# Kernel tuning notes

Measured on AMD Instinct MI355X. Metric: run time of the kernel, lower is better.

The kernel has to match this reference:

```python
import jax, jax.numpy as jnp
import numpy as np

B, T, TA = 16, 512, 1024
D_REG, D_AUD, HID, HEADS = 512, 512, 256, 4
NREG = 4  # mouth, left_eye, right_eye, nose (dict order)
N = NREG * B * T + B * TA  # total graph nodes


def _build_edges():
    # Faithful, vectorized version of build_graph's edge construction (phoneme_times=None).
    bs = np.arange(B)[:, None]
    ts = np.arange(T)[None, :]
    src, dst = [], []
    # cross-region same-timestep edges, all ordered pairs i != j (edge_attr 0)
    for i in range(NREG):
        for j in range(NREG):
            if i != j:
                n1 = i * B * T + bs * T + ts
                n2 = j * B * T + bs * T + ts
                src.append(n1.ravel()); dst.append(n2.ravel())
    # temporal edges within each region (edge_attr 1)
    tt = np.arange(T - 1)[None, :]
    for i in range(NREG):
        n1 = i * B * T + bs * T + tt
        src.append(n1.ravel()); dst.append((n1 + 1).ravel())
    # eye (region idx 1,2) -> audio alignment edges (edge_attr 3)
    t_aud = (np.arange(T)[None, :] * TA) // T
    audio_start = NREG * B * T
    for i in (1, 2):
        n_eye = i * B * T + bs * T + ts
        n_aud = audio_start + bs * TA + t_aud
        src.append(n_eye.ravel()); dst.append(np.broadcast_to(n_aud, (B, T)).ravel())
    # self loops (PyG GATConv default add_self_loops=True)
    loops = np.arange(N)
    src.append(loops); dst.append(loops)
    return np.concatenate(src).astype(np.int32), np.concatenate(dst).astype(np.int32)


def setup_inputs() -> dict:
    key = jax.random.key(0)
    ks = iter(jax.random.split(key, 48))
    def rn(shape, scale=1.0):
        return jax.random.normal(next(ks), shape, dtype=jnp.float32) * jnp.float32(scale)
    src_np, dst_np = _build_edges()
    inp = {
        'mouth': rn((B, T, D_REG)), 'left_eye': rn((B, T, D_REG)),
        'right_eye': rn((B, T, D_REG)), 'nose': rn((B, T, D_REG)),
        'audio_embeddings': rn((B, TA, D_AUD)),
    }
    s = 1.0 / np.sqrt(D_REG)
    for name in ['mouth', 'left_eye', 'right_eye', 'nose']:
        inp['w_' + name] = rn((D_REG, HID), s)
        inp['b_' + name] = jnp.zeros((HID,), jnp.float32)
    inp['w_audio'] = rn((D_AUD, HID), 1.0 / np.sqrt(D_AUD))
    inp['b_audio'] = jnp.zeros((HID,), jnp.float32)
    # GAT layers: layer 0 in=HID, layers 1,2 in=HID*HEADS; layers 0,1 concat, layer 2 averages heads
    dims_in = [HID, HID * HEADS, HID * HEADS]
    for l, din in enumerate(dims_in):
        concat = l < 2
        inp[f'W{l}'] = rn((din, HEADS * HID), 1.0 / np.sqrt(din))
        inp[f'as{l}'] = rn((HEADS, HID), 0.1)
        inp[f'ad{l}'] = rn((HEADS, HID), 0.1)
        inp[f'bias{l}'] = jnp.zeros((HEADS * HID,) if concat else (HID,), jnp.float32)
    inp['ln_g'] = jnp.ones((HID,), jnp.float32)
    inp['ln_b'] = jnp.zeros((HID,), jnp.float32)
    inp['src'] = jnp.asarray(src_np)
    inp['dst'] = jnp.asarray(dst_np)
    return inp


def _gat(x, W, a_s, a_d, bias, src, dst, concat):
    # PyG GATConv (eval mode): gather -> per-head attention softmax over dst -> scatter-add
    H, C = a_s.shape
    h = (x @ W).reshape(-1, H, C)                      # [N,H,C]
    alpha_s = jnp.sum(h * a_s, -1)                     # [N,H]
    alpha_d = jnp.sum(h * a_d, -1)                     # [N,H]
    e = jax.nn.leaky_relu(alpha_s[src] + alpha_d[dst], 0.2)  # [E,H]
    m = jax.ops.segment_max(e, dst, num_segments=N)
    ex = jnp.exp(e - m[dst])
    denom = jax.ops.segment_sum(ex, dst, num_segments=N)
    alpha = ex / (denom[dst] + jnp.float32(1e-16))
    out = jax.ops.segment_sum(h[src] * alpha[:, :, None], dst, num_segments=N)  # [N,H,C]
    out = out.reshape(-1, H * C) if concat else out.mean(1)
    return out + bias


def _forward(mouth, left_eye, right_eye, nose, audio_embeddings,
             w_mouth, b_mouth, w_left_eye, b_left_eye, w_right_eye, b_right_eye,
             w_nose, b_nose, w_audio, b_audio,
             W0, as0, ad0, bias0, W1, as1, ad1, bias1, W2, as2, ad2, bias2,
             ln_g, ln_b, src, dst):
    x = jnp.concatenate([
        (mouth @ w_mouth + b_mouth).reshape(B * T, HID),
        (left_eye @ w_left_eye + b_left_eye).reshape(B * T, HID),
        (right_eye @ w_right_eye + b_right_eye).reshape(B * T, HID),
        (nose @ w_nose + b_nose).reshape(B * T, HID),
        (audio_embeddings @ w_audio + b_audio).reshape(B * TA, HID),
    ], axis=0)                                          # [N,HID]
    x = _gat(x, W0, as0, ad0, bias0, src, dst, True)    # [N,HID*HEADS]
    x = _gat(x, W1, as1, ad1, bias1, src, dst, True)    # [N,HID*HEADS]
    x = _gat(x, W2, as2, ad2, bias2, src, dst, False)   # [N,HID]
    mu = x.mean(-1, keepdims=True)
    var = jnp.mean(jnp.square(x - mu), -1, keepdims=True)
    x = (x - mu) / jnp.sqrt(var + jnp.float32(1e-5)) * ln_g + ln_b
    nodes_pb = NREG * T + TA
    return x.reshape(B, nodes_pb, HID).mean(1)          # [B,HID]


def reference(mouth, left_eye, right_eye, nose, audio_embeddings,
              w_mouth, b_mouth, w_left_eye, b_left_eye, w_right_eye, b_right_eye,
              w_nose, b_nose, w_audio, b_audio,
              W0, as0, ad0, bias0, W1, as1, ad1, bias1, W2, as2, ad2, bias2,
              ln_g, ln_b, src, dst):
    return _forward(mouth, left_eye, right_eye, nose, audio_embeddings,
                    w_mouth, b_mouth, w_left_eye, b_left_eye, w_right_eye, b_right_eye,
                    w_nose, b_nose, w_audio, b_audio,
                    W0, as0, ad0, bias0, W1, as1, ad1, bias1, W2, as2, ad2, bias2,
                    ln_g, ln_b, src, dst)
```

## Files before the change

kernel.cpp:

```cpp
#include <hip/hip_runtime.h>


typedef unsigned short u16;
typedef unsigned int u32;
typedef __bf16 bf16x8 __attribute__((ext_vector_type(8)));
typedef float f32x4 __attribute__((ext_vector_type(4)));

#define ASYNC16(gp, lp)                                                        \
  __builtin_amdgcn_global_load_lds(                                            \
      (const __attribute__((address_space(1))) void*)(gp),                     \
      (__attribute__((address_space(3))) void*)(lp), 16, 0, 0)

__device__ __forceinline__ u16 f2bf(float f) {
  union { float f; u32 u; } v; v.f = f;
  u32 u = v.u + 0x7FFFu + ((v.u >> 16) & 1u);
  return (u16)(u >> 16);
}
__device__ __forceinline__ float bf2f(u16 x) {
  union { u32 u; float f; } v; v.u = ((u32)x) << 16;
  return v.f;
}
__device__ __forceinline__ float4 cvt4(ushort4 s) {
  float4 r; r.x = bf2f(s.x); r.y = bf2f(s.y); r.z = bf2f(s.z); r.w = bf2f(s.w);
  return r;
}
__device__ __forceinline__ float4 load_bf4(const u16* p) {
  return cvt4(*(const ushort4*)p);
}
__device__ __forceinline__ float lrelu(float v) { return v > 0.f ? v : 0.2f * v; }
__device__ __forceinline__ float dot4(float4 a, float4 b) {
  return a.x * b.x + a.y * b.y + a.z * b.z + a.w * b.w;
}
__device__ __forceinline__ float wredx(float v) {
#pragma unroll
  for (int off = 32; off; off >>= 1) v += __shfl_xor(v, off);
  return v;
}

struct PK { const float* W[8]; u16* P[8]; int KB[8]; int NN[8]; int st[9]; };
__global__ __launch_bounds__(256) void pack_kernel(PK p) {
  const int f = blockIdx.x * 4 + (threadIdx.x >> 6);
  const int lane = threadIdx.x & 63;
  int e = 0;
  while (f >= p.st[e + 1]) ++e;
  const int local = f - p.st[e];
  const int KB = p.KB[e], N = p.NN[e];
  const int nt = local / KB, kb = local % KB;
  const float* W = p.W[e] + (size_t)(kb * 32 + (lane >> 4) * 8) * N + nt * 16 + (lane & 15);
  u16* dst = p.P[e] + ((size_t)local * 64 + lane) * 8;
  u16 o[8];
#pragma unroll
  for (int j = 0; j < 8; ++j) o[j] = f2bf(W[(size_t)j * N]);
  *(uint4*)dst = *(uint4*)o;
}

__global__ __launch_bounds__(256) void gemm_kernel(
    const u16* __restrict__ A, const u16* __restrict__ Bp, u16* __restrict__ C,
    int K, int ldc) {
  __shared__ __align__(16) u16 As[2][2][128 * 32];
  const int KB = K >> 5;
  const int KB2 = K >> 6;
  const int w = blockIdx.y * 8 + blockIdx.x;
  const int xcd = w & 7, m = w >> 3;
  const int blockCol = (m & 7) * 128;
  const int blockRow = ((m >> 3) * 8 + xcd) * 128;
  const int tid = threadIdx.x;
  const int wave = tid >> 6, lane = tid & 63;
  const int wr = (wave >> 1) * 64, wc = (wave & 1) * 64;
  const int lr = lane & 15, lq = lane >> 4;
  const int sRow = wave * 16 + (lane >> 2);
  const int sGc = (lane & 3) ^ ((sRow >> 1) & 3);
  const size_t aOff0 = (size_t)(blockRow + sRow) * K + sGc * 8;
  const size_t aOff1 = aOff0 + (size_t)64 * K;
  const int ldsOff0 = wave * 512;
  const int ldsOff1 = 2048 + wave * 512;

  const u16* Bn[4];
#pragma unroll
  for (int ni = 0; ni < 4; ++ni)
    Bn[ni] = Bp + ((size_t)(((blockCol + wc) >> 4) + ni) * KB) * 512 + lane * 8;

  f32x4 acc[4][4] = {};

#pragma unroll
  for (int h = 0; h < 2; ++h) {
    ASYNC16(A + aOff0 + h * 32, As[0][h] + ldsOff0);
    ASYNC16(A + aOff1 + h * 32, As[0][h] + ldsOff1);
  }
  __syncthreads();

  for (int kb2 = 0; kb2 < KB2; ++kb2) {
    const int cb = kb2 & 1;
    if (kb2 + 1 < KB2) {
      const size_t k1 = (size_t)(kb2 + 1) * 64;
#pragma unroll
      for (int h = 0; h < 2; ++h) {
        ASYNC16(A + aOff0 + k1 + h * 32, As[cb ^ 1][h] + ldsOff0);
        ASYNC16(A + aOff1 + k1 + h * 32, As[cb ^ 1][h] + ldsOff1);
      }
    }
#pragma unroll
    for (int h = 0; h < 2; ++h) {
      const int kb = kb2 * 2 + h;
      const u16* cur = As[cb][h];
      bf16x8 bfr[4];
#pragma unroll
      for (int ni = 0; ni < 4; ++ni)
        bfr[ni] = *(const bf16x8*)(Bn[ni] + (size_t)kb * 512);
      bf16x8 af[4];
#pragma unroll
      for (int mi = 0; mi < 4; ++mi) {
        const int R = wr + mi * 16 + lr;
        const int cp = lq ^ ((R >> 1) & 3);
        af[mi] = *(const bf16x8*)(cur + R * 32 + cp * 8);
      }
#pragma unroll
      for (int mi = 0; mi < 4; ++mi)
#pragma unroll
        for (int ni = 0; ni < 4; ++ni)
          acc[mi][ni] = __builtin_amdgcn_mfma_f32_16x16x32_bf16(af[mi], bfr[ni],
                                                                acc[mi][ni], 0, 0, 0);
    }
    __syncthreads();
  }
#pragma unroll
  for (int mi = 0; mi < 4; ++mi)
#pragma unroll
    for (int ni = 0; ni < 4; ++ni) {
      const int col = blockCol + wc + ni * 16 + lr;
#pragma unroll
      for (int r = 0; r < 4; ++r) {
        const int row = blockRow + wr + mi * 16 + lq * 4 + r;
        C[(size_t)row * ldc + col] = f2bf(acc[mi][ni][r]);
      }
    }
}

struct ProjArgs { const float* x[5]; const u16* w[5]; const float* b[5]; };
__global__ __launch_bounds__(256) void proj_kernel(ProjArgs pa,
                                                   u16* __restrict__ C) {
  __shared__ __align__(16) u16 As[128 * 32];
  const int blockRow = blockIdx.y * 128, blockCol = blockIdx.x * 128;
  const int reg = blockRow >= 32768 ? 4 : (blockRow >> 13);
  const int regBase = reg == 4 ? 32768 : reg * 8192;
  const float* Af = pa.x[reg] + (size_t)(blockRow - regBase) * 512;
  const u16* Bp = pa.w[reg];
  const int tid = threadIdx.x;
  const int wave = tid >> 6, lane = tid & 63;
  const int wr = (wave >> 1) * 64, wc = (wave & 1) * 64;
  const int lr = lane & 15, lq = lane >> 4;
  const int rr = tid >> 2;
  const int cphys = tid & 3;
  const int sGc = cphys ^ ((tid >> 3) & 3);

  const u16* Bn[4];
#pragma unroll
  for (int ni = 0; ni < 4; ++ni)
    Bn[ni] = Bp + ((size_t)(((blockCol + wc) >> 4) + ni) * 16) * 512 + lane * 8;

  f32x4 acc[4][4] = {};

  for (int k0 = 0; k0 < 512; k0 += 32) {
    __syncthreads();
    bf16x8 bfr[4];
#pragma unroll
    for (int ni = 0; ni < 4; ++ni)
      bfr[ni] = *(const bf16x8*)(Bn[ni] + (size_t)k0 * 16);
#pragma unroll
    for (int i = 0; i < 2; ++i) {
      const int row = i * 64 + rr;
      const float* ap = Af + (size_t)row * 512 + k0 + sGc * 8;
      float4 f0 = *(const float4*)(ap);
      float4 f1 = *(const float4*)(ap + 4);
      uint4 pk;
      pk.x = (u32)f2bf(f0.x) | ((u32)f2bf(f0.y) << 16);
      pk.y = (u32)f2bf(f0.z) | ((u32)f2bf(f0.w) << 16);
      pk.z = (u32)f2bf(f1.x) | ((u32)f2bf(f1.y) << 16);
      pk.w = (u32)f2bf(f1.z) | ((u32)f2bf(f1.w) << 16);
      *(uint4*)(&As[row * 32 + cphys * 8]) = pk;
    }
    __syncthreads();
    bf16x8 af[4];
#pragma unroll
    for (int mi = 0; mi < 4; ++mi) {
      const int R = wr + mi * 16 + lr;
      const int cp = lq ^ ((R >> 1) & 3);
      af[mi] = *(const bf16x8*)(&As[R * 32 + cp * 8]);
    }
#pragma unroll
    for (int mi = 0; mi < 4; ++mi)
#pragma unroll
      for (int ni = 0; ni < 4; ++ni)
        acc[mi][ni] = __builtin_amdgcn_mfma_f32_16x16x32_bf16(af[mi], bfr[ni],
                                                              acc[mi][ni], 0, 0, 0);
  }
  const float* bias = pa.b[reg];
#pragma unroll
  for (int mi = 0; mi < 4; ++mi)
#pragma unroll
    for (int ni = 0; ni < 4; ++ni) {
      const int col = blockCol + wc + ni * 16 + lr;
      const float bv = bias[col];
#pragma unroll
      for (int r = 0; r < 4; ++r) {
        const int row = blockRow + wr + mi * 16 + lq * 4 + r;
        C[(size_t)row * 256 + col] = f2bf(acc[mi][ni][r] + bv);
      }
    }
}

template <bool MEAN>
__global__ __launch_bounds__(256) void agg_kernel(
    const u16* __restrict__ h, const float* __restrict__ a_s,
    const float* __restrict__ a_d, const float* __restrict__ bias,
    const float* __restrict__ lng, const float* __restrict__ lnb,
    void* __restrict__ out) {
  const int tid = threadIdx.x;
  const int head = tid >> 6;
  const int c4 = tid * 4;
  const float4 sa = *(const float4*)(a_s + c4);
  const float4 da = *(const float4*)(a_d + c4);

  if (blockIdx.x < 2048) {
    const int b = blockIdx.x >> 7;
    const int t0 = (blockIdx.x & 127) * 4;
    const int btBase = b * 512 + t0;
    float4 hprev[4];
    float ssPrev[4] = {};
    if (t0 > 0) {
#pragma unroll
      for (int r = 0; r < 4; ++r)
        hprev[r] = load_bf4(h + (size_t)(r * 8192 + btBase - 1) * 1024 + c4);
#pragma unroll
      for (int r = 0; r < 4; ++r) ssPrev[r] = wredx(dot4(hprev[r], sa));
    }
    ushort4 rcur[4];
#pragma unroll
    for (int r = 0; r < 4; ++r)
      rcur[r] = *(const ushort4*)(h + (size_t)(r * 8192 + btBase) * 1024 + c4);

    float pacc[4] = {};
    int pch[4] = {-1, -1, -1, -1};

    for (int tt = 0; tt < 4; ++tt) {
      const int bt = btBase + tt;
      const bool hasPrev = (t0 + tt) > 0;
      ushort4 rnxt[4];
      if (tt < 3) {
#pragma unroll
        for (int r = 0; r < 4; ++r)
          rnxt[r] = *(const ushort4*)(h + (size_t)(r * 8192 + bt + 1) * 1024 + c4);
      }
      float4 hv[4];
#pragma unroll
      for (int r = 0; r < 4; ++r) hv[r] = cvt4(rcur[r]);
      float ss[4], dd[4];
#pragma unroll
      for (int r = 0; r < 4; ++r) {
        ss[r] = wredx(dot4(hv[r], sa));
        dd[r] = wredx(dot4(hv[r], da));
      }
      float4 av[4];
#pragma unroll
      for (int j = 0; j < 4; ++j) {
        const float ad = dd[j];
        float e0 = lrelu(ss[0] + ad), e1 = lrelu(ss[1] + ad);
        float e2 = lrelu(ss[2] + ad), e3 = lrelu(ss[3] + ad);
        float mx = fmaxf(fmaxf(e0, e1), fmaxf(e2, e3));
        float e4 = 0.f;
        if (hasPrev) { e4 = lrelu(ssPrev[j] + ad); mx = fmaxf(mx, e4); }
        const float x0 = __expf(e0 - mx), x1 = __expf(e1 - mx);
        const float x2 = __expf(e2 - mx), x3 = __expf(e3 - mx);
        const float x4 = hasPrev ? __expf(e4 - mx) : 0.f;
        const float inv = 1.f / (x0 + x1 + x2 + x3 + x4 + 1e-16f);
        const float a0 = x0 * inv, a1 = x1 * inv, a2 = x2 * inv, a3 = x3 * inv;
        const float a4 = x4 * inv;
        float4 acc;
        acc.x = a0 * hv[0].x + a1 * hv[1].x + a2 * hv[2].x + a3 * hv[3].x;
        acc.y = a0 * hv[0].y + a1 * hv[1].y + a2 * hv[2].y + a3 * hv[3].y;
        acc.z = a0 * hv[0].z + a1 * hv[1].z + a2 * hv[2].z + a3 * hv[3].z;
        acc.w = a0 * hv[0].w + a1 * hv[1].w + a2 * hv[2].w + a3 * hv[3].w;
        if (hasPrev) {
          acc.x += a4 * hprev[j].x; acc.y += a4 * hprev[j].y;
          acc.z += a4 * hprev[j].z; acc.w += a4 * hprev[j].w;
        }
        av[j] = acc;
      }
      if constexpr (!MEAN) {
        const float4 bv = *(const float4*)(bias + c4);
        u16* ob = (u16*)out;
#pragma unroll
        for (int j = 0; j < 4; ++j) {
          ushort4 o;
          o.x = f2bf(av[j].x + bv.x); o.y = f2bf(av[j].y + bv.y);
          o.z = f2bf(av[j].z + bv.z); o.w = f2bf(av[j].w + bv.w);
          *(ushort4*)(ob + (size_t)(j * 8192 + bt) * 1024 + c4) = o;
        }
      } else {
        __shared__ float red[4096];
        __shared__ float ls[32];
#pragma unroll
        for (int j = 0; j < 4; ++j) *(float4*)(&red[j * 1024 + c4]) = av[j];
        __syncthreads();
        const float bb = bias[tid];
        float v[4];
#pragma unroll
        for (int j = 0; j < 4; ++j) {
          v[j] = 0.25f * (red[j * 1024 + tid] + red[j * 1024 + tid + 256] +
                          red[j * 1024 + tid + 512] + red[j * 1024 + tid + 768]) + bb;
          const float sj = wredx(v[j]);
          const float qj = wredx(v[j] * v[j]);
          if ((tid & 63) == 0) { ls[head * 8 + j * 2] = sj; ls[head * 8 + j * 2 + 1] = qj; }
        }
        __syncthreads();
#pragma unroll
        for (int j = 0; j < 4; ++j) {
          const float S = ls[j * 2] + ls[8 + j * 2] + ls[16 + j * 2] + ls[24 + j * 2];
          const float Q = ls[j * 2 + 1] + ls[8 + j * 2 + 1] + ls[16 + j * 2 + 1] +
                          ls[24 + j * 2 + 1];
          const float mean = S * (1.f / 256.f);
          const float var = Q * (1.f / 256.f) - mean * mean;
          const float n = (v[j] - mean) * rsqrtf(var + 1e-5f) * lng[tid] + lnb[tid];
          const int ch = (j * 8192 + bt) / 3072;
          if (ch != pch[j]) {
            if (pch[j] >= 0) atomicAdd((float*)out + pch[j] * 256 + tid, pacc[j]);
            pacc[j] = 0.f; pch[j] = ch;
          }
          pacc[j] += n;
        }
      }
#pragma unroll
      for (int r = 0; r < 4; ++r) {
        hprev[r] = hv[r];
        ssPrev[r] = ss[r];
        rcur[r] = rnxt[r];
      }
    }
    if constexpr (MEAN) {
#pragma unroll
      for (int j = 0; j < 4; ++j)
        if (pch[j] >= 0) atomicAdd((float*)out + pch[j] * 256 + tid, pacc[j]);
    }
  } else {
    const int aid = blockIdx.x - 2048;
    const int idx0 = aid * 2;
    const int b = idx0 >> 10;
    const int ta0 = idx0 & 1023;
    const int n0 = 32768 + idx0, n1 = n0 + 1;
    const int tt2 = ta0 >> 1;
    const int le = 8192 + b * 512 + tt2;
    const int re = 16384 + b * 512 + tt2;
    float4 v0 = load_bf4(h + (size_t)n0 * 1024 + c4);
    float4 vo = load_bf4(h + (size_t)n1 * 1024 + c4);
    float4 v1 = load_bf4(h + (size_t)le * 1024 + c4);
    float4 v2 = load_bf4(h + (size_t)re * 1024 + c4);
    const float s0 = wredx(dot4(v0, sa));
    const float s1 = wredx(dot4(v1, sa));
    const float s2 = wredx(dot4(v2, sa));
    const float d0 = wredx(dot4(v0, da));
    {
      const float e0 = lrelu(s0 + d0), e1 = lrelu(s1 + d0), e2 = lrelu(s2 + d0);
      const float mx = fmaxf(e0, fmaxf(e1, e2));
      const float x0 = __expf(e0 - mx), x1 = __expf(e1 - mx), x2 = __expf(e2 - mx);
      const float inv = 1.f / (x0 + x1 + x2 + 1e-16f);
      const float a0 = x0 * inv, a1 = x1 * inv, a2 = x2 * inv;
      v0.x = a0 * v0.x + a1 * v1.x + a2 * v2.x;
      v0.y = a0 * v0.y + a1 * v1.y + a2 * v2.y;
      v0.z = a0 * v0.z + a1 * v1.z + a2 * v2.z;
      v0.w = a0 * v0.w + a1 * v1.w + a2 * v2.w;
    }
    if constexpr (!MEAN) {
      const float4 bv = *(const float4*)(bias + c4);
      ushort4 oe, oo;
      oe.x = f2bf(v0.x + bv.x); oe.y = f2bf(v0.y + bv.y);
      oe.z = f2bf(v0.z + bv.z); oe.w = f2bf(v0.w + bv.w);
      oo.x = f2bf(vo.x + bv.x); oo.y = f2bf(vo.y + bv.y);
      oo.z = f2bf(vo.z + bv.z); oo.w = f2bf(vo.w + bv.w);
      *(ushort4*)((u16*)out + (size_t)n0 * 1024 + c4) = oe;
      *(ushort4*)((u16*)out + (size_t)n1 * 1024 + c4) = oo;
    } else {
      __shared__ float redA[2048];
      __shared__ float lsA[32];
      *(float4*)(&redA[c4]) = v0;
      *(float4*)(&redA[1024 + c4]) = vo;
      __syncthreads();
      const float bb = bias[tid];
      float vA = 0.25f * (redA[tid] + redA[tid + 256] + redA[tid + 512] +
                          redA[tid + 768]) + bb;
      float vB = 0.25f * (redA[1024 + tid] + redA[1024 + tid + 256] +
                          redA[1024 + tid + 512] + redA[1024 + tid + 768]) + bb;
      const float sA = wredx(vA), qA = wredx(vA * vA);
      const float sB = wredx(vB), qB = wredx(vB * vB);
      if ((tid & 63) == 0) {
        lsA[head * 8] = sA; lsA[head * 8 + 1] = qA;
        lsA[head * 8 + 2] = sB; lsA[head * 8 + 3] = qB;
      }
      __syncthreads();
      const float SA = lsA[0] + lsA[8] + lsA[16] + lsA[24];
      const float QA = lsA[1] + lsA[9] + lsA[17] + lsA[25];
      const float SB = lsA[2] + lsA[10] + lsA[18] + lsA[26];
      const float QB = lsA[3] + lsA[11] + lsA[19] + lsA[27];
      const float mA = SA * (1.f / 256.f), vrA = QA * (1.f / 256.f) - mA * mA;
      const float mB = SB * (1.f / 256.f), vrB = QB * (1.f / 256.f) - mB * mB;
      const float g = lng[tid], be = lnb[tid];
      const float nA = (vA - mA) * rsqrtf(vrA + 1e-5f) * g + be;
      const float nB = (vB - mB) * rsqrtf(vrB + 1e-5f) * g + be;
      const int ch0 = n0 / 3072, ch1 = n1 / 3072;
      if (ch0 == ch1) {
        atomicAdd((float*)out + ch0 * 256 + tid, nA + nB);
      } else {
        atomicAdd((float*)out + ch0 * 256 + tid, nA);
        atomicAdd((float*)out + ch1 * 256 + tid, nB);
      }
    }
  }
}

__global__ __launch_bounds__(256) void zero_kernel(float* __restrict__ p) {
  p[blockIdx.x * 256 + threadIdx.x] = 0.f;
}
__global__ __launch_bounds__(256) void scale_kernel(float* __restrict__ p) {
  const int i = blockIdx.x * 256 + threadIdx.x;
  p[i] *= (1.f / 3072.f);
}

extern "C" void kernel_launch(void* const* d_in, const int* in_sizes, int n_in,
                              void* d_out, int out_size, void* d_ws, size_t ws_size,
                              hipStream_t stream) {
  const float* x_reg[4] = {(const float*)d_in[0], (const float*)d_in[1],
                           (const float*)d_in[2], (const float*)d_in[3]};
  const float* audio = (const float*)d_in[4];
  const float* w_reg[4] = {(const float*)d_in[5], (const float*)d_in[7],
                           (const float*)d_in[9], (const float*)d_in[11]};
  const float* b_reg[4] = {(const float*)d_in[6], (const float*)d_in[8],
                           (const float*)d_in[10], (const float*)d_in[12]};
  const float* w_aud = (const float*)d_in[13];
  const float* b_aud = (const float*)d_in[14];
  const float* Wl[3] = {(const float*)d_in[15], (const float*)d_in[19],
                        (const float*)d_in[23]};
  const float* as_in[3] = {(const float*)d_in[16], (const float*)d_in[20],
                           (const float*)d_in[24]};
  const float* ad_in[3] = {(const float*)d_in[17], (const float*)d_in[21],
                           (const float*)d_in[25]};
  const float* bias_l[3] = {(const float*)d_in[18], (const float*)d_in[22],
                            (const float*)d_in[26]};
  const float* ln_g = (const float*)d_in[27];
  const float* ln_b = (const float*)d_in[28];

  char* ws = (char*)d_ws;
  u16* h_bf = (u16*)ws;
  u16* xb = (u16*)(ws + 100663296);
  u16* wt = (u16*)(ws + 201326592);

  u16* wtp[5];
  for (int r = 0; r < 5; ++r) wtp[r] = wt + (size_t)r * 131072;
  u16* wt0 = wt + 655360;
  u16* wt1 = wt + 917504;
  u16* wt2 = wt + 1966080;

  PK pk;
  for (int r = 0; r < 4; ++r) { pk.W[r] = w_reg[r]; pk.P[r] = wtp[r]; pk.KB[r] = 16; pk.NN[r] = 256; }
  pk.W[4] = w_aud; pk.P[4] = wtp[4]; pk.KB[4] = 16; pk.NN[4] = 256;
  pk.W[5] = Wl[0]; pk.P[5] = wt0; pk.KB[5] = 8;  pk.NN[5] = 1024;
  pk.W[6] = Wl[1]; pk.P[6] = wt1; pk.KB[6] = 32; pk.NN[6] = 1024;
  pk.W[7] = Wl[2]; pk.P[7] = wt2; pk.KB[7] = 32; pk.NN[7] = 1024;
  pk.st[0] = 0;
  {
    const int nfr[8] = {256, 256, 256, 256, 256, 512, 2048, 2048};
    int acc = 0;
    for (int e = 0; e < 8; ++e) { acc += nfr[e]; pk.st[e + 1] = acc; }
  }
  pack_kernel<<<pk.st[8] / 4, 256, 0, stream>>>(pk);
  zero_kernel<<<16, 256, 0, stream>>>((float*)d_out);

  ProjArgs pa;
  for (int r = 0; r < 4; ++r) { pa.x[r] = x_reg[r]; pa.w[r] = wtp[r]; pa.b[r] = b_reg[r]; }
  pa.x[4] = audio; pa.w[4] = wtp[4]; pa.b[4] = b_aud;
  proj_kernel<<<dim3(2, 384), 256, 0, stream>>>(pa, xb);

  const u16* wl[3] = {wt0, wt1, wt2};
  const int Kl[3] = {256, 1024, 1024};
  for (int l = 0; l < 3; ++l) {
    gemm_kernel<<<dim3(8, 384), 256, 0, stream>>>(xb, wl[l], h_bf, Kl[l], 1024);
    if (l < 2)
      agg_kernel<false><<<10240, 256, 0, stream>>>(h_bf, as_in[l], ad_in[l],
                                                   bias_l[l], nullptr, nullptr, xb);
    else
      agg_kernel<true><<<10240, 256, 0, stream>>>(h_bf, as_in[l], ad_in[l],
                                                  bias_l[l], ln_g, ln_b, d_out);
  }

  scale_kernel<<<16, 256, 0, stream>>>((float*)d_out);
}
```

Measured before the change: 710.7 us.

## Assign one timestep per aggregation block and spread mean atomics across slots

The aggregation kernel now gives each block a single (batch,timestep) for the region nodes and a single audio node, replacing the 4-timestep sequential loop and paired audio nodes. This raises the grid from 10240 to 24576 blocks to expose more parallelism, at the cost of reloading each previous-timestep row instead of carrying it in registers. The final mean now accumulates into 8 partial slots per batch to cut atomic contention, and a finish kernel sums the slots and applies the scaling. Shared memory for the mean variant is moved to a dynamic allocation.

```diff
diff --git a/kernel.cpp b/kernel.cpp
--- a/kernel.cpp
+++ b/kernel.cpp
@@ -23,9 +23,6 @@
 __device__ __forceinline__ float4 cvt4(ushort4 s) {
   float4 r; r.x = bf2f(s.x); r.y = bf2f(s.y); r.z = bf2f(s.z); r.w = bf2f(s.w);
   return r;
-}
-__device__ __forceinline__ float4 load_bf4(const u16* p) {
-  return cvt4(*(const ushort4*)p);
 }
 __device__ __forceinline__ float lrelu(float v) { return v > 0.f ? v : 0.2f * v; }
 __device__ __forceinline__ float dot4(float4 a, float4 b) {
@@ -215,203 +212,158 @@
     const float* __restrict__ a_d, const float* __restrict__ bias,
     const float* __restrict__ lng, const float* __restrict__ lnb,
     void* __restrict__ out) {
+  extern __shared__ float dyn[];
   const int tid = threadIdx.x;
   const int head = tid >> 6;
   const int c4 = tid * 4;
   const float4 sa = *(const float4*)(a_s + c4);
   const float4 da = *(const float4*)(a_d + c4);
 
-  if (blockIdx.x < 2048) {
-    const int b = blockIdx.x >> 7;
-    const int t0 = (blockIdx.x & 127) * 4;
-    const int btBase = b * 512 + t0;
-    float4 hprev[4];
-    float ssPrev[4] = {};
-    if (t0 > 0) {
+  if (blockIdx.x < 8192) {
+    const int bt = blockIdx.x;
+    const int t = bt & 511;
+    const bool hasPrev = t > 0;
+    ushort4 rv[4], rp[4];
+#pragma unroll
+    for (int r = 0; r < 4; ++r)
+      rv[r] = *(const ushort4*)(h + (size_t)(r * 8192 + bt) * 1024 + c4);
+    if (hasPrev) {
 #pragma unroll
       for (int r = 0; r < 4; ++r)
-        hprev[r] = load_bf4(h + (size_t)(r * 8192 + btBase - 1) * 1024 + c4);
-#pragma unroll
-      for (int r = 0; r < 4; ++r) ssPrev[r] = wredx(dot4(hprev[r], sa));
-    }
-    ushort4 rcur[4];
-#pragma unroll
-    for (int r = 0; r < 4; ++r)
-      rcur[r] = *(const ushort4*)(h + (size_t)(r * 8192 + btBase) * 1024 + c4);
-
-    float pacc[4] = {};
-    int pch[4] = {-1, -1, -1, -1};
-
-    for (int tt = 0; tt < 4; ++tt) {
-      const int bt = btBase + tt;
-      const bool hasPrev = (t0 + tt) > 0;
-      ushort4 rnxt[4];
-      if (tt < 3) {
-#pragma unroll
-        for (int r = 0; r < 4; ++r)
-          rnxt[r] = *(const ushort4*)(h + (size_t)(r * 8192 + bt + 1) * 1024 + c4);
-      }
-      float4 hv[4];
-#pragma unroll
-      for (int r = 0; r < 4; ++r) hv[r] = cvt4(rcur[r]);
-      float ss[4], dd[4];
-#pragma unroll
-      for (int r = 0; r < 4; ++r) {
-        ss[r] = wredx(dot4(hv[r], sa));
-        dd[r] = wredx(dot4(hv[r], da));
-      }
-      float4 av[4];
+        rp[r] = *(const ushort4*)(h + (size_t)(r * 8192 + bt - 1) * 1024 + c4);
+    }
+    float4 hv[4], hp[4];
+#pragma unroll
+    for (int r = 0; r < 4; ++r) hv[r] = cvt4(rv[r]);
+    float ss[4], dd[4], sp[4];
+#pragma unroll
+    for (int r = 0; r < 4; ++r) {
+      ss[r] = wredx(dot4(hv[r], sa));
+      dd[r] = wredx(dot4(hv[r], da));
+    }
+    if (hasPrev) {
+#pragma unroll
+      for (int r = 0; r < 4; ++r) hp[r] = cvt4(rp[r]);
+#pragma unroll
+      for (int r = 0; r < 4; ++r) sp[r] = wredx(dot4(hp[r], sa));
+    }
+    float4 av[4];
+#pragma unroll
+    for (int j = 0; j < 4; ++j) {
+      const float ad = dd[j];
+      float e0 = lrelu(ss[0] + ad), e1 = lrelu(ss[1] + ad);
+      float e2 = lrelu(ss[2] + ad), e3 = lrelu(ss[3] + ad);
+      float mx = fmaxf(fmaxf(e0, e1), fmaxf(e2, e3));
+      float e4 = 0.f;
+      if (hasPrev) { e4 = lrelu(sp[j] + ad); mx = fmaxf(mx, e4); }
+      const float x0 = __expf(e0 - mx), x1 = __expf(e1 - mx);
+      const float x2 = __expf(e2 - mx), x3 = __expf(e3 - mx);
+      const float x4 = hasPrev ? __expf(e4 - mx) : 0.f;
+      const float inv = 1.f / (x0 + x1 + x2 + x3 + x4 + 1e-16f);
+      const float a0 = x0 * inv, a1 = x1 * inv, a2 = x2 * inv, a3 = x3 * inv;
+      const float a4 = x4 * inv;
+      float4 acc;
+      acc.x = a0 * hv[0].x + a1 * hv[1].x + a2 * hv[2].x + a3 * hv[3].x;
+      acc.y = a0 * hv[0].y + a1 * hv[1].y + a2 * hv[2].y + a3 * hv[3].y;
+      acc.z = a0 * hv[0].z + a1 * hv[1].z + a2 * hv[2].z + a3 * hv[3].z;
+      acc.w = a0 * hv[0].w + a1 * hv[1].w + a2 * hv[2].w + a3 * hv[3].w;
+      if (hasPrev) {
+        acc.x += a4 * hp[j].x; acc.y += a4 * hp[j].y;
+        acc.z += a4 * hp[j].z; acc.w += a4 * hp[j].w;
+      }
+      av[j] = acc;
+    }
+    if constexpr (!MEAN) {
+      const float4 bv = *(const float4*)(bias + c4);
+      u16* ob = (u16*)out;
 #pragma unroll
       for (int j = 0; j < 4; ++j) {
-        const float ad = dd[j];
-        float e0 = lrelu(ss[0] + ad), e1 = lrelu(ss[1] + ad);
-        float e2 = lrelu(ss[2] + ad), e3 = lrelu(ss[3] + ad);
-        float mx = fmaxf(fmaxf(e0, e1), fmaxf(e2, e3));
-        float e4 = 0.f;
-        if (hasPrev) { e4 = lrelu(ssPrev[j] + ad); mx = fmaxf(mx, e4); }
-        const float x0 = __expf(e0 - mx), x1 = __expf(e1 - mx);
-        const float x2 = __expf(e2 - mx), x3 = __expf(e3 - mx);
-        const float x4 = hasPrev ? __expf(e4 - mx) : 0.f;
-        const float inv = 1.f / (x0 + x1 + x2 + x3 + x4 + 1e-16f);
-        const float a0 = x0 * inv, a1 = x1 * inv, a2 = x2 * inv, a3 = x3 * inv;
-        const float a4 = x4 * inv;
-        float4 acc;
-        acc.x = a0 * hv[0].x + a1 * hv[1].x + a2 * hv[2].x + a3 * hv[3].x;
-        acc.y = a0 * hv[0].y + a1 * hv[1].y + a2 * hv[2].y + a3 * hv[3].y;
-        acc.z = a0 * hv[0].z + a1 * hv[1].z + a2 * hv[2].z + a3 * hv[3].z;
-        acc.w = a0 * hv[0].w + a1 * hv[1].w + a2 * hv[2].w + a3 * hv[3].w;
-        if (hasPrev) {
-          acc.x += a4 * hprev[j].x; acc.y += a4 * hprev[j].y;
-          acc.z += a4 * hprev[j].z; acc.w += a4 * hprev[j].w;
-        }
-        av[j] = acc;
-      }
-      if constexpr (!MEAN) {
-        const float4 bv = *(const float4*)(bias + c4);
-        u16* ob = (u16*)out;
-#pragma unroll
-        for (int j = 0; j < 4; ++j) {
-          ushort4 o;
-          o.x = f2bf(av[j].x + bv.x); o.y = f2bf(av[j].y + bv.y);
-          o.z = f2bf(av[j].z + bv.z); o.w = f2bf(av[j].w + bv.w);
-          *(ushort4*)(ob + (size_t)(j * 8192 + bt) * 1024 + c4) = o;
-        }
-      } else {
-        __shared__ float red[4096];
-        __shared__ float ls[32];
-#pragma unroll
-        for (int j = 0; j < 4; ++j) *(float4*)(&red[j * 1024 + c4]) = av[j];
-        __syncthreads();
-        const float bb = bias[tid];
-        float v[4];
-#pragma unroll
-        for (int j = 0; j < 4; ++j) {
-          v[j] = 0.25f * (red[j * 1024 + tid] + red[j * 1024 + tid + 256] +
-                          red[j * 1024 + tid + 512] + red[j * 1024 + tid + 768]) + bb;
-          const float sj = wredx(v[j]);
-          const float qj = wredx(v[j] * v[j]);
-          if ((tid & 63) == 0) { ls[head * 8 + j * 2] = sj; ls[head * 8 + j * 2 + 1] = qj; }
-        }
-        __syncthreads();
-#pragma unroll
-        for (int j = 0; j < 4; ++j) {
-          const float S = ls[j * 2] + ls[8 + j * 2] + ls[16 + j * 2] + ls[24 + j * 2];
-          const float Q = ls[j * 2 + 1] + ls[8 + j * 2 + 1] + ls[16 + j * 2 + 1] +
-                          ls[24 + j * 2 + 1];
-          const float mean = S * (1.f / 256.f);
-          const float var = Q * (1.f / 256.f) - mean * mean;
-          const float n = (v[j] - mean) * rsqrtf(var + 1e-5f) * lng[tid] + lnb[tid];
-          const int ch = (j * 8192 + bt) / 3072;
-          if (ch != pch[j]) {
-            if (pch[j] >= 0) atomicAdd((float*)out + pch[j] * 256 + tid, pacc[j]);
-            pacc[j] = 0.f; pch[j] = ch;
-          }
-          pacc[j] += n;
-        }
-      }
-#pragma unroll
-      for (int r = 0; r < 4; ++r) {
-        hprev[r] = hv[r];
-        ssPrev[r] = ss[r];
-        rcur[r] = rnxt[r];
-      }
-    }
-    if constexpr (MEAN) {
-#pragma unroll
-      for (int j = 0; j < 4; ++j)
-        if (pch[j] >= 0) atomicAdd((float*)out + pch[j] * 256 + tid, pacc[j]);
+        ushort4 o;
+        o.x = f2bf(av[j].x + bv.x); o.y = f2bf(av[j].y + bv.y);
+        o.z = f2bf(av[j].z + bv.z); o.w = f2bf(av[j].w + bv.w);
+        *(ushort4*)(ob + (size_t)(j * 8192 + bt) * 1024 + c4) = o;
+      }
+    } else {
+      float* red = dyn;
+      float* ls = dyn + 4096;
+#pragma unroll
+      for (int j = 0; j < 4; ++j) *(float4*)(&red[j * 1024 + c4]) = av[j];
+      __syncthreads();
+      const float bb = bias[tid];
+      float v[4];
+#pragma unroll
+      for (int j = 0; j < 4; ++j) {
+        v[j] = 0.25f * (red[j * 1024 + tid] + red[j * 1024 + tid + 256] +
+                        red[j * 1024 + tid + 512] + red[j * 1024 + tid + 768]) + bb;
+        const float sj = wredx(v[j]);
+        const float qj = wredx(v[j] * v[j]);
+        if ((tid & 63) == 0) { ls[head * 8 + j * 2] = sj; ls[head * 8 + j * 2 + 1] = qj; }
+      }
+      __syncthreads();
+      const int slot = bt & 7;
+      float* po = (float*)out;
+#pragma unroll
+      for (int j = 0; j < 4; ++j) {
+        const float S = ls[j * 2] + ls[8 + j * 2] + ls[16 + j * 2] + ls[24 + j * 2];
+        const float Q = ls[j * 2 + 1] + ls[8 + j * 2 + 1] + ls[16 + j * 2 + 1] +
+                        ls[24 + j * 2 + 1];
+        const float mean = S * (1.f / 256.f);
+        const float var = Q * (1.f / 256.f) - mean * mean;
+        const float n = (v[j] - mean) * rsqrtf(var + 1e-5f) * lng[tid] + lnb[tid];
+        const int ch = (j * 8192 + bt) / 3072;
+        atomicAdd(po + (ch * 8 + slot) * 256 + tid, n);
+      }
     }
   } else {
-    const int aid = blockIdx.x - 2048;
-    const int idx0 = aid * 2;
-    const int b = idx0 >> 10;
-    const int ta0 = idx0 & 1023;
-    const int n0 = 32768 + idx0, n1 = n0 + 1;
-    const int tt2 = ta0 >> 1;
-    const int le = 8192 + b * 512 + tt2;
-    const int re = 16384 + b * 512 + tt2;
-    float4 v0 = load_bf4(h + (size_t)n0 * 1024 + c4);
-    float4 vo = load_bf4(h + (size_t)n1 * 1024 + c4);
-    float4 v1 = load_bf4(h + (size_t)le * 1024 + c4);
-    float4 v2 = load_bf4(h + (size_t)re * 1024 + c4);
-    const float s0 = wredx(dot4(v0, sa));
-    const float s1 = wredx(dot4(v1, sa));
-    const float s2 = wredx(dot4(v2, sa));
-    const float d0 = wredx(dot4(v0, da));
-    {
+    const int idx = blockIdx.x - 8192;
+    const int ta = idx & 1023;
+    const int node = 32768 + idx;
+    const bool even = ((ta & 1) == 0);
+    float4 v = cvt4(*(const ushort4*)(h + (size_t)node * 1024 + c4));
+    if (even) {
+      const int b = idx >> 10;
+      const int tt = ta >> 1;
+      const int le = 8192 + b * 512 + tt;
+      const int re = 16384 + b * 512 + tt;
+      float4 v1 = cvt4(*(const ushort4*)(h + (size_t)le * 1024 + c4));
+      float4 v2 = cvt4(*(const ushort4*)(h + (size_t)re * 1024 + c4));
+      const float s0 = wredx(dot4(v, sa));
+      const float s1 = wredx(dot4(v1, sa));
+      const float s2 = wredx(dot4(v2, sa));
+      const float d0 = wredx(dot4(v, da));
       const float e0 = lrelu(s0 + d0), e1 = lrelu(s1 + d0), e2 = lrelu(s2 + d0);
       const float mx = fmaxf(e0, fmaxf(e1, e2));
       const float x0 = __expf(e0 - mx), x1 = __expf(e1 - mx), x2 = __expf(e2 - mx);
       const float inv = 1.f / (x0 + x1 + x2 + 1e-16f);
       const float a0 = x0 * inv, a1 = x1 * inv, a2 = x2 * inv;
-      v0.x = a0 * v0.x + a1 * v1.x + a2 * v2.x;
-      v0.y = a0 * v0.y + a1 * v1.y + a2 * v2.y;
-      v0.z = a0 * v0.z + a1 * v1.z + a2 * v2.z;
-      v0.w = a0 * v0.w + a1 * v1.w + a2 * v2.w;
+      v.x = a0 * v.x + a1 * v1.x + a2 * v2.x;
+      v.y = a0 * v.y + a1 * v1.y + a2 * v2.y;
+      v.z = a0 * v.z + a1 * v1.z + a2 * v2.z;
+      v.w = a0 * v.w + a1 * v1.w + a2 * v2.w;
     }
     if constexpr (!MEAN) {
       const float4 bv = *(const float4*)(bias + c4);
-      ushort4 oe, oo;
-      oe.x = f2bf(v0.x + bv.x); oe.y = f2bf(v0.y + bv.y);
-      oe.z = f2bf(v0.z + bv.z); oe.w = f2bf(v0.w + bv.w);
-      oo.x = f2bf(vo.x + bv.x); oo.y = f2bf(vo.y + bv.y);
-      oo.z = f2bf(vo.z + bv.z); oo.w = f2bf(vo.w + bv.w);
-      *(ushort4*)((u16*)out + (size_t)n0 * 1024 + c4) = oe;
-      *(ushort4*)((u16*)out + (size_t)n1 * 1024 + c4) = oo;
+      ushort4 o;
+      o.x = f2bf(v.x + bv.x); o.y = f2bf(v.y + bv.y);
+      o.z = f2bf(v.z + bv.z); o.w = f2bf(v.w + bv.w);
+      *(ushort4*)((u16*)out + (size_t)node * 1024 + c4) = o;
     } else {
-      __shared__ float redA[2048];
-      __shared__ float lsA[32];
-      *(float4*)(&redA[c4]) = v0;
-      *(float4*)(&redA[1024 + c4]) = vo;
+      float* red = dyn;
+      float* ls = dyn + 4096;
+      *(float4*)(&red[c4]) = v;
       __syncthreads();
-      const float bb = bias[tid];
-      float vA = 0.25f * (redA[tid] + redA[tid + 256] + redA[tid + 512] +
-                          redA[tid + 768]) + bb;
-      float vB = 0.25f * (redA[1024 + tid] + redA[1024 + tid + 256] +
-                          redA[1024 + tid + 512] + redA[1024 + tid + 768]) + bb;
+      float vA = 0.25f * (red[tid] + red[tid + 256] + red[tid + 512] +
+                          red[tid + 768]) + bias[tid];
       const float sA = wredx(vA), qA = wredx(vA * vA);
-      const float sB = wredx(vB), qB = wredx(vB * vB);
-      if ((tid & 63) == 0) {
-        lsA[head * 8] = sA; lsA[head * 8 + 1] = qA;
-        lsA[head * 8 + 2] = sB; lsA[head * 8 + 3] = qB;
-      }
+      if ((tid & 63) == 0) { ls[head * 2] = sA; ls[head * 2 + 1] = qA; }
       __syncthreads();
-      const float SA = lsA[0] + lsA[8] + lsA[16] + lsA[24];
-      const float QA = lsA[1] + lsA[9] + lsA[17] + lsA[25];
-      const float SB = lsA[2] + lsA[10] + lsA[18] + lsA[26];
-      const float QB = lsA[3] + lsA[11] + lsA[19] + lsA[27];
-      const float mA = SA * (1.f / 256.f), vrA = QA * (1.f / 256.f) - mA * mA;
-      const float mB = SB * (1.f / 256.f), vrB = QB * (1.f / 256.f) - mB * mB;
-      const float g = lng[tid], be = lnb[tid];
-      const float nA = (vA - mA) * rsqrtf(vrA + 1e-5f) * g + be;
-      const float nB = (vB - mB) * rsqrtf(vrB + 1e-5f) * g + be;
-      const int ch0 = n0 / 3072, ch1 = n1 / 3072;
-      if (ch0 == ch1) {
-        atomicAdd((float*)out + ch0 * 256 + tid, nA + nB);
-      } else {
-        atomicAdd((float*)out + ch0 * 256 + tid, nA);
-        atomicAdd((float*)out + ch1 * 256 + tid, nB);
-      }
+      const float S = ls[0] + ls[2] + ls[4] + ls[6];
+      const float Q = ls[1] + ls[3] + ls[5] + ls[7];
+      const float mean = S * (1.f / 256.f);
+      const float var = Q * (1.f / 256.f) - mean * mean;
+      const float n = (vA - mean) * rsqrtf(var + 1e-5f) * lng[tid] + lnb[tid];
+      const int ch = node / 3072;
+      atomicAdd((float*)out + (ch * 8 + (idx & 7)) * 256 + tid, n);
     }
   }
 }
@@ -419,9 +371,14 @@
 __global__ __launch_bounds__(256) void zero_kernel(float* __restrict__ p) {
   p[blockIdx.x * 256 + threadIdx.x] = 0.f;
 }
-__global__ __launch_bounds__(256) void scale_kernel(float* __restrict__ p) {
-  const int i = blockIdx.x * 256 + threadIdx.x;
-  p[i] *= (1.f / 3072.f);
+__global__ __launch_bounds__(256) void finish_kernel(const float* __restrict__ part,
+                                                     float* __restrict__ out) {
+  const int chunk = blockIdx.x;
+  const int c = threadIdx.x;
+  float s = 0.f;
+#pragma unroll
+  for (int k = 0; k < 8; ++k) s += part[(chunk * 8 + k) * 256 + c];
+  out[chunk * 256 + c] = s * (1.f / 3072.f);
 }
 
 extern "C" void kernel_launch(void* const* d_in, const int* in_sizes, int n_in,
@@ -451,6 +408,7 @@
   u16* h_bf = (u16*)ws;
   u16* xb = (u16*)(ws + 100663296);
   u16* wt = (u16*)(ws + 201326592);
+  float* part = (float*)(ws + 207355904);
 
   u16* wtp[5];
   for (int r = 0; r < 5; ++r) wtp[r] = wt + (size_t)r * 131072;
@@ -471,7 +429,7 @@
     for (int e = 0; e < 8; ++e) { acc += nfr[e]; pk.st[e + 1] = acc; }
   }
   pack_kernel<<<pk.st[8] / 4, 256, 0, stream>>>(pk);
-  zero_kernel<<<16, 256, 0, stream>>>((float*)d_out);
+  zero_kernel<<<128, 256, 0, stream>>>(part);
 
   ProjArgs pa;
   for (int r = 0; r < 4; ++r) { pa.x[r] = x_reg[r]; pa.w[r] = wtp[r]; pa.b[r] = b_reg[r]; }
@@ -480,15 +438,16 @@
 
   const u16* wl[3] = {wt0, wt1, wt2};
   const int Kl[3] = {256, 1024, 1024};
+  const size_t dynLds = (4096 + 32) * sizeof(float);
   for (int l = 0; l < 3; ++l) {
     gemm_kernel<<<dim3(8, 384), 256, 0, stream>>>(xb, wl[l], h_bf, Kl[l], 1024);
     if (l < 2)
-      agg_kernel<false><<<10240, 256, 0, stream>>>(h_bf, as_in[l], ad_in[l],
+      agg_kernel<false><<<24576, 256, 0, stream>>>(h_bf, as_in[l], ad_in[l],
                                                    bias_l[l], nullptr, nullptr, xb);
     else
-      agg_kernel<true><<<10240, 256, 0, stream>>>(h_bf, as_in[l], ad_in[l],
-                                                  bias_l[l], ln_g, ln_b, d_out);
-  }
-
-  scale_kernel<<<16, 256, 0, stream>>>((float*)d_out);
-}
+      agg_kernel<true><<<24576, 256, dynLds, stream>>>(h_bf, as_in[l], ad_in[l],
+                                                       bias_l[l], ln_g, ln_b, part);
+  }
+
+  finish_kernel<<<16, 256, 0, stream>>>(part, (float*)d_out);
+}
```

Result: faster. 690.0 us (-2.9%).
